# Optimization experiments

Measured on AMD Instinct MI355X. Metric: run time of the kernel, lower is better.

Reference implementation:

```python
import jax, jax.numpy as jnp
import numpy as np

DIM = 1024
CTX_DIM = 1024
HEADS = 8
DIM_HEAD = 64
INNER = HEADS * DIM_HEAD  # 512
EPS = 1e-5


def _layer_norm(x, gamma, beta):
    mu = jnp.mean(x, axis=-1, keepdims=True)
    var = jnp.mean(jnp.square(x - mu), axis=-1, keepdims=True)
    return (x - mu) * jax.lax.rsqrt(var + EPS) * gamma + beta


def setup_inputs() -> dict:
    key = jax.random.key(0)
    ks = jax.random.split(key, 8)
    b, n, m = 4, 2048, 2048
    x = jax.random.normal(ks[0], (b, n, DIM), dtype=jnp.float32)
    context = jax.random.normal(ks[1], (b, m, CTX_DIM), dtype=jnp.float32)
    Wq = jax.random.normal(ks[2], (DIM, INNER), dtype=jnp.float32) / np.sqrt(DIM)
    Wkv = jax.random.normal(ks[3], (CTX_DIM, 2 * INNER), dtype=jnp.float32) / np.sqrt(CTX_DIM)
    Wout = jax.random.normal(ks[4], (INNER, DIM), dtype=jnp.float32) / np.sqrt(INNER)
    bout = jnp.zeros((DIM,), dtype=jnp.float32)
    g1 = jnp.ones((DIM,), dtype=jnp.float32)
    b1 = jnp.zeros((DIM,), dtype=jnp.float32)
    g2 = jnp.ones((CTX_DIM,), dtype=jnp.float32)
    b2 = jnp.zeros((CTX_DIM,), dtype=jnp.float32)
    return {"x": x, "context": context, "g1": g1, "b1": b1, "g2": g2, "b2": b2,
            "Wq": Wq, "Wkv": Wkv, "Wout": Wout, "bout": bout}


def reference(x, context, g1, b1, g2, b2, Wq, Wkv, Wout, bout):
    b, n, _ = x.shape
    m = context.shape[1]
    scale = DIM_HEAD ** -0.5
    xn = _layer_norm(x, g1, b1)
    cn = _layer_norm(context, g2, b2)
    q = xn @ Wq                      # [b, n, inner]
    kv = cn @ Wkv                    # [b, m, 2*inner]
    k, v = jnp.split(kv, 2, axis=-1)
    # split heads: [b, h, seq, d]
    q = q.reshape(b, n, HEADS, DIM_HEAD).transpose(0, 2, 1, 3)
    k = k.reshape(b, m, HEADS, DIM_HEAD).transpose(0, 2, 1, 3)
    v = v.reshape(b, m, HEADS, DIM_HEAD).transpose(0, 2, 1, 3)
    sim = jnp.einsum('bhid,bhjd->bhij', q, k) * scale
    attn = jax.nn.softmax(sim, axis=-1)
    out = jnp.einsum('bhij,bhjd->bhid', attn, v)
    out = out.transpose(0, 2, 1, 3).reshape(b, n, INNER)
    return out @ Wout + bout
```

## Files before the change

kernel.cpp:

```cpp
#include <hip/hip_runtime.h>
#include <hip/hip_bf16.h>

typedef __bf16 bf16_t;
typedef bf16_t bf16x4 __attribute__((ext_vector_type(4)));
typedef bf16_t bf16x8 __attribute__((ext_vector_type(8)));
typedef float floatx4 __attribute__((ext_vector_type(4)));

typedef __attribute__((address_space(1))) const unsigned char* gptr_t;
typedef __attribute__((address_space(3))) unsigned char* lptr_t;

#define BATCH 4
#define SEQ_N 2048
#define SEQ_M 2048
#define DIM 1024
#define INNER 512
#define HEADS 8
#define DHEAD 64
#define QSCALE 0.18033688011112042f

#if __has_builtin(__builtin_amdgcn_exp2f)
#define fast_exp2(x) __builtin_amdgcn_exp2f(x)
#else
#define fast_exp2(x) exp2f(x)
#endif

__device__ __forceinline__ void wtrans_tile(const float* W, bf16_t* Wt,
                                            int K, int N, int n0, int k0, float scale) {
    __shared__ bf16_t T[64][72];
    const int tid = threadIdx.x;
#pragma unroll
    for (int p = 0; p < 2; p++) {
        int r = (tid >> 3) + p * 32;
        int c = (tid & 7) * 8;
        const float* src = W + (size_t)(k0 + r) * N + n0 + c;
        float4 v0 = *(const float4*)src;
        float4 v1 = *(const float4*)(src + 4);
        T[r][c + 0] = (bf16_t)(v0.x * scale); T[r][c + 1] = (bf16_t)(v0.y * scale);
        T[r][c + 2] = (bf16_t)(v0.z * scale); T[r][c + 3] = (bf16_t)(v0.w * scale);
        T[r][c + 4] = (bf16_t)(v1.x * scale); T[r][c + 5] = (bf16_t)(v1.y * scale);
        T[r][c + 6] = (bf16_t)(v1.z * scale); T[r][c + 7] = (bf16_t)(v1.w * scale);
    }
    __syncthreads();
#pragma unroll
    for (int p = 0; p < 2; p++) {
        int rn = (tid >> 3) + p * 32;
        int ck = (tid & 7) * 8;
        bf16x8 v;
#pragma unroll
        for (int i = 0; i < 8; i++) v[i] = T[ck + i][rn];
        *(bf16x8*)(Wt + (size_t)(n0 + rn) * K + k0 + ck) = v;
    }
}

__device__ __forceinline__ void ln_row_wave(const float* in, const float* g,
                                            const float* bt, bf16_t* out, int row) {
    const int lane = threadIdx.x & 63;
    const float4* src = (const float4*)(in + (size_t)row * 1024);
    float4 xv[4];
    float s = 0.f, ss = 0.f;
#pragma unroll
    for (int k = 0; k < 4; k++) {
        xv[k] = src[lane + k * 64];
        s  += xv[k].x + xv[k].y + xv[k].z + xv[k].w;
        ss += xv[k].x * xv[k].x + xv[k].y * xv[k].y + xv[k].z * xv[k].z + xv[k].w * xv[k].w;
    }
#pragma unroll
    for (int off = 32; off > 0; off >>= 1) {
        s  += __shfl_down(s, off);
        ss += __shfl_down(ss, off);
    }
    s  = __shfl(s, 0);
    ss = __shfl(ss, 0);
    const float mu = s * (1.f / 1024.f);
    const float var = ss * (1.f / 1024.f) - mu * mu;
    const float rs = rsqrtf(var + 1e-5f);
    const float4* gp = (const float4*)g;
    const float4* bp = (const float4*)bt;
#pragma unroll
    for (int k = 0; k < 4; k++) {
        float4 gv = gp[lane + k * 64], bv = bp[lane + k * 64];
        bf16x4 o;
        o[0] = (bf16_t)((xv[k].x - mu) * rs * gv.x + bv.x);
        o[1] = (bf16_t)((xv[k].y - mu) * rs * gv.y + bv.y);
        o[2] = (bf16_t)((xv[k].z - mu) * rs * gv.z + bv.z);
        o[3] = (bf16_t)((xv[k].w - mu) * rs * gv.w + bv.w);
        *(bf16x4*)(out + (size_t)row * 1024 + (lane + k * 64) * 4) = o;
    }
}

__global__ __launch_bounds__(256) void prep_kernel(const float* __restrict__ x,
                                                   const float* __restrict__ ctx,
                                                   const float* __restrict__ g1,
                                                   const float* __restrict__ b1,
                                                   const float* __restrict__ g2,
                                                   const float* __restrict__ b2,
                                                   const float* __restrict__ Wq,
                                                   const float* __restrict__ Wkv,
                                                   const float* __restrict__ Wout,
                                                   bf16_t* __restrict__ xn,
                                                   bf16_t* __restrict__ cn,
                                                   bf16_t* __restrict__ Wqt,
                                                   bf16_t* __restrict__ Wkvt,
                                                   bf16_t* __restrict__ Woutt) {
    int id = blockIdx.x;
    if (id < 128) {
        wtrans_tile(Wq, Wqt, 1024, 512, (id & 7) * 64, (id >> 3) * 64, QSCALE);
    } else if (id < 384) {
        int t = id - 128;
        wtrans_tile(Wkv, Wkvt, 1024, 1024, (t & 15) * 64, (t >> 4) * 64, 1.0f);
    } else if (id < 512) {
        int t = id - 384;
        wtrans_tile(Wout, Woutt, 512, 1024, (t & 15) * 64, (t >> 4) * 64, 1.0f);
    } else {
        int row = (id - 512) * 4 + (threadIdx.x >> 6);
        if (row < BATCH * SEQ_N) ln_row_wave(x, g1, b1, xn, row);
        else                     ln_row_wave(ctx, g2, b2, cn, row - BATCH * SEQ_N);
    }
}

template <int NT, int MODE, typename OutT>
__device__ __forceinline__ void gemm_body(const bf16_t* __restrict__ A,
                                          const bf16_t* __restrict__ Bt,
                                          OutT* __restrict__ C,
                                          const float* __restrict__ bias,
                                          int ldC, int K, int row0, int col0) {
    __shared__ bf16_t As[128 * 64];
    __shared__ bf16_t Bs[NT * 64];
    const int tid = threadIdx.x;
    const int wave = tid >> 6, lane = tid & 63;
    constexpr int WC = NT / 2;
    constexpr int NJ = WC / 16;
    const int wr = (wave >> 1) * 64, wc = (wave & 1) * WC;
    const int quad = lane >> 4, l16 = lane & 15;

    floatx4 acc[4][NJ] = {};

    for (int k0 = 0; k0 < K; k0 += 64) {
#pragma unroll
        for (int p = 0; p < 4; p++) {
            int cA = p * 256 + wave * 64 + lane;
            int rA = cA >> 3, kc = (cA & 7) * 8;
            __builtin_amdgcn_global_load_lds(
                (gptr_t)(A + (size_t)(row0 + rA) * K + k0 + kc),
                (lptr_t)(As + (size_t)(p * 256 + wave * 64) * 8), 16, 0, 0);
            if (p < NT / 32)
                __builtin_amdgcn_global_load_lds(
                    (gptr_t)(Bt + (size_t)(col0 + rA) * K + k0 + kc),
                    (lptr_t)(Bs + (size_t)(p * 256 + wave * 64) * 8), 16, 0, 0);
        }
        __syncthreads();
#pragma unroll
        for (int kt = 0; kt < 2; kt++) {
            bf16x8 aF[4], bF[NJ];
#pragma unroll
            for (int i = 0; i < 4; i++)
                aF[i] = *(bf16x8*)&As[(wr + i * 16 + l16) * 64 + kt * 32 + quad * 8];
#pragma unroll
            for (int j = 0; j < NJ; j++)
                bF[j] = *(bf16x8*)&Bs[(wc + j * 16 + l16) * 64 + kt * 32 + quad * 8];
#pragma unroll
            for (int i = 0; i < 4; i++)
#pragma unroll
                for (int j = 0; j < NJ; j++) {
                    if (MODE == 0)
                        acc[i][j] = __builtin_amdgcn_mfma_f32_16x16x32_bf16(
                            aF[i], bF[j], acc[i][j], 0, 0, 0);
                    else
                        acc[i][j] = __builtin_amdgcn_mfma_f32_16x16x32_bf16(
                            bF[j], aF[i], acc[i][j], 0, 0, 0);
                }
        }
        __syncthreads();
    }

    if (MODE == 0) {
#pragma unroll
        for (int i = 0; i < 4; i++)
#pragma unroll
            for (int j = 0; j < NJ; j++) {
                int col = col0 + wc + j * 16 + l16;
                float bv = bias ? bias[col] : 0.f;
#pragma unroll
                for (int r = 0; r < 4; r++) {
                    int row = row0 + wr + i * 16 + quad * 4 + r;
                    C[(size_t)row * ldC + col] = (OutT)(acc[i][j][r] + bv);
                }
            }
    } else {
        bf16_t* Tw = (wave < 2 ? As : Bs) + (wave & 1) * 4096;
#pragma unroll
        for (int i = 0; i < 4; i++)
#pragma unroll
            for (int j = 0; j < 4; j++)
#pragma unroll
                for (int r = 0; r < 4; r++)
                    Tw[(j * 16 + quad * 4 + r) * 64 + i * 16 + l16] = (bf16_t)acc[i][j][r];
        __syncthreads();
        const int grow = row0 + wr;
        const int bat = grow >> 11, gm = (grow & 2047) + l16 * 4;
#pragma unroll
        for (int dd = 0; dd < 16; dd++) {
            int d = dd * 4 + quad;
            bf16x4 v = *(bf16x4*)&Tw[d * 64 + l16 * 4];
            int gd = col0 + wc + d - 512;
            *(bf16x4*)(C + ((size_t)bat * 512 + gd) * 2048 + gm) = v;
        }
    }
}

__global__ __launch_bounds__(256) void gemm_qkv_kernel(const bf16_t* __restrict__ xn,
                                                       const bf16_t* __restrict__ cn,
                                                       const bf16_t* __restrict__ Wqt,
                                                       const bf16_t* __restrict__ Wkvt,
                                                       bf16_t* __restrict__ qb,
                                                       bf16_t* __restrict__ kvb,
                                                       bf16_t* __restrict__ Vtg) {
    const int bx = blockIdx.x;
    const int row0 = blockIdx.y * 128;
    if (bx < 4)
        gemm_body<128, 0, bf16_t>(xn, Wqt, qb, nullptr, 512, DIM, row0, bx * 128);
    else if (bx < 8)
        gemm_body<128, 0, bf16_t>(cn, Wkvt, kvb, nullptr, 512, DIM, row0, (bx - 4) * 128);
    else
        gemm_body<128, 1, bf16_t>(cn, Wkvt, Vtg, nullptr, 0, DIM, row0, (bx - 4) * 128);
}

__global__ __launch_bounds__(256) void gemm_out_kernel(const bf16_t* __restrict__ ao,
                                                       const bf16_t* __restrict__ Woutt,
                                                       float* __restrict__ out,
                                                       const float* __restrict__ bias) {
    gemm_body<64, 0, float>(ao, Woutt, out, bias, DIM, INNER,
                            blockIdx.y * 128, blockIdx.x * 64);
}

__global__ __launch_bounds__(128) void attn_kernel(const bf16_t* __restrict__ q,
                                                   const bf16_t* __restrict__ kv,
                                                   const bf16_t* __restrict__ Vtg,
                                                   bf16_t* __restrict__ o) {
    __shared__ bf16_t Qs[64 * 64];
    __shared__ bf16_t Ks[2][64 * 64];
    __shared__ bf16_t Vs[2][64 * 64];

    const int f = blockIdx.x;
    const int lb = ((f & 7) << 7) | (f >> 3);
    const int b = lb >> 8, h = (lb >> 5) & 7;
    const int n0 = (lb & 31) * 64;

    const int tid = threadIdx.x;
    const int wave = tid >> 6, lane = tid & 63;
    const int quad = lane >> 4, l16 = lane & 15;
    const int swz = (l16 & 7) << 3;

    const int sr = tid >> 3;
    const int sc = (tid & 7) * 8;
    const int scs = sc ^ ((sr & 7) << 3);

#pragma unroll
    for (int p = 0; p < 4; p++) {
        int r = sr + p * 16;
        *(bf16x8*)&Qs[r * 64 + scs] =
            *(const bf16x8*)(q + (size_t)(b * SEQ_N + n0 + r) * INNER + h * DHEAD + sc);
    }

    bf16x8 bOnes;
    {
        bf16_t ov = (l16 == 0) ? (bf16_t)1.0f : (bf16_t)0.0f;
#pragma unroll
        for (int i = 0; i < 8; i++) bOnes[i] = ov;
    }

    const bf16_t* kp = kv + (size_t)(b * SEQ_M) * 512 + h * DHEAD + sc;
    const bf16_t* vp = Vtg + (size_t)((b * HEADS + h) * DHEAD) * SEQ_M + sc;
    bf16x8 kreg[4], vreg[4];
#pragma unroll
    for (int p = 0; p < 4; p++) {
        kreg[p] = *(const bf16x8*)(kp + (size_t)(sr + p * 16) * 512);
        vreg[p] = *(const bf16x8*)(vp + (size_t)(sr + p * 16) * SEQ_M);
    }
    __syncthreads();

    bf16x8 aQ0[2], aQ1[2];
#pragma unroll
    for (int kt = 0; kt < 2; kt++) {
        aQ0[kt] = *(bf16x8*)&Qs[(wave * 32 + l16) * 64 + ((kt * 32 + quad * 8) ^ swz)];
        aQ1[kt] = *(bf16x8*)&Qs[(wave * 32 + 16 + l16) * 64 + ((kt * 32 + quad * 8) ^ swz)];
    }

#pragma unroll
    for (int p = 0; p < 4; p++) {
        int r = sr + p * 16;
        *(bf16x8*)&Ks[0][r * 64 + scs] = kreg[p];
        *(bf16x8*)&Vs[0][r * 64 + scs] = vreg[p];
    }
    kp += 64 * 512;
    vp += 64;
#pragma unroll
    for (int p = 0; p < 4; p++) {
        kreg[p] = *(const bf16x8*)(kp + (size_t)(sr + p * 16) * 512);
        vreg[p] = *(const bf16x8*)(vp + (size_t)(sr + p * 16) * SEQ_M);
    }
    __syncthreads();

    bf16_t* Pw0 = Qs + wave * 2048;
    bf16_t* Pw1 = Pw0 + 1024;

    floatx4 oacc0[5] = {}, oacc1[5] = {};

    int cur = 0;
    for (int it = 0; it < SEQ_M / 64; ++it) {
#pragma unroll
        for (int p = 0; p < 4; p++) {
            int r = sr + p * 16;
            *(bf16x8*)&Ks[cur ^ 1][r * 64 + scs] = kreg[p];
            *(bf16x8*)&Vs[cur ^ 1][r * 64 + scs] = vreg[p];
        }
        kp += 64 * 512;
        vp += 64;
#pragma unroll
        for (int p = 0; p < 4; p++) {
            kreg[p] = *(const bf16x8*)(kp + (size_t)(sr + p * 16) * 512);
            vreg[p] = *(const bf16x8*)(vp + (size_t)(sr + p * 16) * SEQ_M);
        }

        floatx4 s0[4] = {}, s1[4] = {};
#pragma unroll
        for (int kt = 0; kt < 2; kt++)
#pragma unroll
            for (int jt = 0; jt < 4; jt++) {
                bf16x8 aK = *(bf16x8*)&Ks[cur][(jt * 16 + l16) * 64 +
                                              ((kt * 32 + quad * 8) ^ swz)];
                s0[jt] = __builtin_amdgcn_mfma_f32_16x16x32_bf16(aK, aQ0[kt], s0[jt], 0, 0, 0);
                s1[jt] = __builtin_amdgcn_mfma_f32_16x16x32_bf16(aK, aQ1[kt], s1[jt], 0, 0, 0);
            }

#pragma unroll
        for (int jt = 0; jt < 4; jt++) {
            bf16x4 pk0, pk1;
#pragma unroll
            for (int r = 0; r < 4; r++) {
                pk0[r] = (bf16_t)fast_exp2(s0[jt][r]);
                pk1[r] = (bf16_t)fast_exp2(s1[jt][r]);
            }
            int pc = (jt * 16 + quad * 4) ^ swz;
            *(bf16x4*)&Pw0[l16 * 64 + pc] = pk0;
            *(bf16x4*)&Pw1[l16 * 64 + pc] = pk1;
        }

#pragma unroll
        for (int kt = 0; kt < 2; kt++) {
            int ac = (kt * 32 + quad * 8) ^ swz;
            bf16x8 aP0 = *(bf16x8*)&Pw0[l16 * 64 + ac];
            bf16x8 aP1 = *(bf16x8*)&Pw1[l16 * 64 + ac];
#pragma unroll
            for (int dt = 0; dt < 4; dt++) {
                bf16x8 bV = *(bf16x8*)&Vs[cur][(dt * 16 + l16) * 64 + ac];
                oacc0[dt] = __builtin_amdgcn_mfma_f32_16x16x32_bf16(aP0, bV, oacc0[dt], 0, 0, 0);
                oacc1[dt] = __builtin_amdgcn_mfma_f32_16x16x32_bf16(aP1, bV, oacc1[dt], 0, 0, 0);
            }
            oacc0[4] = __builtin_amdgcn_mfma_f32_16x16x32_bf16(aP0, bOnes, oacc0[4], 0, 0, 0);
            oacc1[4] = __builtin_amdgcn_mfma_f32_16x16x32_bf16(aP1, bOnes, oacc1[4], 0, 0, 0);
        }
        __syncthreads();
        cur ^= 1;
    }

#pragma unroll
    for (int set = 0; set < 2; set++) {
        const floatx4* oa = set == 0 ? oacc0 : oacc1;
        float inv[4];
#pragma unroll
        for (int r = 0; r < 4; r++) {
            float l = __shfl(oa[4][r], (int)(lane & 48));
            inv[r] = 1.0f / l;
        }
#pragma unroll
        for (int dt = 0; dt < 4; dt++)
#pragma unroll
            for (int r = 0; r < 4; r++) {
                int row = n0 + wave * 32 + set * 16 + quad * 4 + r;
                int col = h * DHEAD + dt * 16 + l16;
                o[(size_t)(b * SEQ_N + row) * INNER + col] =
                    (bf16_t)(oa[dt][r] * inv[r]);
            }
    }
}

extern "C" void kernel_launch(void* const* d_in, const int* in_sizes, int n_in,
                              void* d_out, int out_size, void* d_ws, size_t ws_size,
                              hipStream_t stream) {
    const float* x    = (const float*)d_in[0];
    const float* ctx  = (const float*)d_in[1];
    const float* g1   = (const float*)d_in[2];
    const float* b1   = (const float*)d_in[3];
    const float* g2   = (const float*)d_in[4];
    const float* b2   = (const float*)d_in[5];
    const float* Wq   = (const float*)d_in[6];
    const float* Wkv  = (const float*)d_in[7];
    const float* Wout = (const float*)d_in[8];
    const float* bout = (const float*)d_in[9];
    float* out = (float*)d_out;

    const int rows = BATCH * SEQ_N;
    bf16_t* xn    = (bf16_t*)d_ws;
    bf16_t* cn    = xn + (size_t)rows * DIM;
    bf16_t* qb    = cn + (size_t)rows * DIM;
    bf16_t* kvb   = qb + (size_t)rows * INNER;
    bf16_t* Vtg   = kvb + (size_t)rows * INNER;
    bf16_t* Wqt   = Vtg + (size_t)rows * INNER;
    bf16_t* Wkvt  = Wqt + (size_t)INNER * DIM;
    bf16_t* Woutt = Wkvt + (size_t)(2 * INNER) * DIM;
    bf16_t* o_attn = xn;

    prep_kernel<<<512 + (2 * rows) / 4, 256, 0, stream>>>(
        x, ctx, g1, b1, g2, b2, Wq, Wkv, Wout, xn, cn, Wqt, Wkvt, Woutt);
    gemm_qkv_kernel<<<dim3(12, rows / 128), 256, 0, stream>>>(
        xn, cn, Wqt, Wkvt, qb, kvb, Vtg);
    attn_kernel<<<dim3(SEQ_N / 64 * HEADS * BATCH), 128, 0, stream>>>(qb, kvb, Vtg, o_attn);
    gemm_out_kernel<<<dim3(DIM / 64, rows / 128), 256, 0, stream>>>(o_attn, Woutt, out, bout);
}
```

Measured before the change: 245.1 us.

## Stream K via direct global-to-LDS loads, read V from global, remap GEMM blocks

The attention kernel now loads K tiles straight into LDS with global_load_lds and an XOR-swizzled source column, replacing the register-staged copy. The V shared buffer is removed: V fragments come from global memory (L2) directly into registers for the PV MFMAs. Both GEMM kernels get 1D grids with XCD-aware block remapping, and attention gets a launch-bounds occupancy hint. This cuts LDS traffic, LDS footprint and register staging, at the cost of V global-load latency inside the loop and reliance on L2 hits.

New measurement: 262.5 us. 1.07x slower.

```diff
diff --git a/kernel.cpp b/kernel.cpp
--- a/kernel.cpp
+++ b/kernel.cpp
@@ -215,8 +215,10 @@
                                                        bf16_t* __restrict__ qb,
                                                        bf16_t* __restrict__ kvb,
                                                        bf16_t* __restrict__ Vtg) {
-    const int bx = blockIdx.x;
-    const int row0 = blockIdx.y * 128;
+    const int f = blockIdx.x;
+    const int lb = (f & 7) * 96 + (f >> 3);
+    const int bx = lb % 12;
+    const int row0 = (lb / 12) * 128;
     if (bx < 4)
         gemm_body<128, 0, bf16_t>(xn, Wqt, qb, nullptr, 512, DIM, row0, bx * 128);
     else if (bx < 8)
@@ -229,17 +231,18 @@
                                                        const bf16_t* __restrict__ Woutt,
                                                        float* __restrict__ out,
                                                        const float* __restrict__ bias) {
+    const int f = blockIdx.x;
+    const int lb = (f & 7) * 128 + (f >> 3);
     gemm_body<64, 0, float>(ao, Woutt, out, bias, DIM, INNER,
-                            blockIdx.y * 128, blockIdx.x * 64);
-}
-
-__global__ __launch_bounds__(128) void attn_kernel(const bf16_t* __restrict__ q,
-                                                   const bf16_t* __restrict__ kv,
-                                                   const bf16_t* __restrict__ Vtg,
-                                                   bf16_t* __restrict__ o) {
+                            (lb >> 4) * 128, (lb & 15) * 64);
+}
+
+__global__ __launch_bounds__(128, 3) void attn_kernel(const bf16_t* __restrict__ q,
+                                                      const bf16_t* __restrict__ kv,
+                                                      const bf16_t* __restrict__ Vtg,
+                                                      bf16_t* __restrict__ o) {
     __shared__ bf16_t Qs[64 * 64];
     __shared__ bf16_t Ks[2][64 * 64];
-    __shared__ bf16_t Vs[2][64 * 64];
 
     const int f = blockIdx.x;
     const int lb = ((f & 7) << 7) | (f >> 3);
@@ -255,6 +258,17 @@
     const int sc = (tid & 7) * 8;
     const int scs = sc ^ ((sr & 7) << 3);
 
+    const int rloc = lane >> 3;
+    const int srccol = ((lane & 7) ^ rloc) << 3;
+    const bf16_t* kgl = kv + ((size_t)(b * SEQ_M) + wave * 32 + rloc) * 512
+                           + h * DHEAD + srccol;
+
+#pragma unroll
+    for (int p = 0; p < 4; p++)
+        __builtin_amdgcn_global_load_lds(
+            (gptr_t)(kgl + (size_t)(p * 8) * 512),
+            (lptr_t)(Ks[0] + (wave * 4 + p) * 512), 16, 0, 0);
+
 #pragma unroll
     for (int p = 0; p < 4; p++) {
         int r = sr + p * 16;
@@ -269,14 +283,6 @@
         for (int i = 0; i < 8; i++) bOnes[i] = ov;
     }
 
-    const bf16_t* kp = kv + (size_t)(b * SEQ_M) * 512 + h * DHEAD + sc;
-    const bf16_t* vp = Vtg + (size_t)((b * HEADS + h) * DHEAD) * SEQ_M + sc;
-    bf16x8 kreg[4], vreg[4];
-#pragma unroll
-    for (int p = 0; p < 4; p++) {
-        kreg[p] = *(const bf16x8*)(kp + (size_t)(sr + p * 16) * 512);
-        vreg[p] = *(const bf16x8*)(vp + (size_t)(sr + p * 16) * SEQ_M);
-    }
     __syncthreads();
 
     bf16x8 aQ0[2], aQ1[2];
@@ -286,20 +292,15 @@
         aQ1[kt] = *(bf16x8*)&Qs[(wave * 32 + 16 + l16) * 64 + ((kt * 32 + quad * 8) ^ swz)];
     }
 
-#pragma unroll
-    for (int p = 0; p < 4; p++) {
-        int r = sr + p * 16;
-        *(bf16x8*)&Ks[0][r * 64 + scs] = kreg[p];
-        *(bf16x8*)&Vs[0][r * 64 + scs] = vreg[p];
-    }
-    kp += 64 * 512;
-    vp += 64;
-#pragma unroll
-    for (int p = 0; p < 4; p++) {
-        kreg[p] = *(const bf16x8*)(kp + (size_t)(sr + p * 16) * 512);
-        vreg[p] = *(const bf16x8*)(vp + (size_t)(sr + p * 16) * SEQ_M);
-    }
-    __syncthreads();
+    kgl += (size_t)64 * 512;
+#pragma unroll
+    for (int p = 0; p < 4; p++)
+        __builtin_amdgcn_global_load_lds(
+            (gptr_t)(kgl + (size_t)(p * 8) * 512),
+            (lptr_t)(Ks[1] + (wave * 4 + p) * 512), 16, 0, 0);
+
+    const bf16_t* vbl =
+        Vtg + ((size_t)((b * HEADS + h) * DHEAD) + l16) * SEQ_M + quad * 8;
 
     bf16_t* Pw0 = Qs + wave * 2048;
     bf16_t* Pw1 = Pw0 + 1024;
@@ -308,20 +309,6 @@
 
     int cur = 0;
     for (int it = 0; it < SEQ_M / 64; ++it) {
-#pragma unroll
-        for (int p = 0; p < 4; p++) {
-            int r = sr + p * 16;
-            *(bf16x8*)&Ks[cur ^ 1][r * 64 + scs] = kreg[p];
-            *(bf16x8*)&Vs[cur ^ 1][r * 64 + scs] = vreg[p];
-        }
-        kp += 64 * 512;
-        vp += 64;
-#pragma unroll
-        for (int p = 0; p < 4; p++) {
-            kreg[p] = *(const bf16x8*)(kp + (size_t)(sr + p * 16) * 512);
-            vreg[p] = *(const bf16x8*)(vp + (size_t)(sr + p * 16) * SEQ_M);
-        }
-
         floatx4 s0[4] = {}, s1[4] = {};
 #pragma unroll
         for (int kt = 0; kt < 2; kt++)
@@ -333,6 +320,11 @@
                 s1[jt] = __builtin_amdgcn_mfma_f32_16x16x32_bf16(aK, aQ1[kt], s1[jt], 0, 0, 0);
             }
 
+        bf16x8 vf0[4], vf1[4];
+#pragma unroll
+        for (int dt = 0; dt < 4; dt++)
+            vf0[dt] = *(const bf16x8*)(vbl + (size_t)(dt * 16) * SEQ_M);
+
 #pragma unroll
         for (int jt = 0; jt < 4; jt++) {
             bf16x4 pk0, pk1;
@@ -347,20 +339,42 @@
         }
 
 #pragma unroll
-        for (int kt = 0; kt < 2; kt++) {
-            int ac = (kt * 32 + quad * 8) ^ swz;
+        for (int dt = 0; dt < 4; dt++)
+            vf1[dt] = *(const bf16x8*)(vbl + (size_t)(dt * 16) * SEQ_M + 32);
+
+        {
+            int ac = (quad * 8) ^ swz;
             bf16x8 aP0 = *(bf16x8*)&Pw0[l16 * 64 + ac];
             bf16x8 aP1 = *(bf16x8*)&Pw1[l16 * 64 + ac];
 #pragma unroll
             for (int dt = 0; dt < 4; dt++) {
-                bf16x8 bV = *(bf16x8*)&Vs[cur][(dt * 16 + l16) * 64 + ac];
-                oacc0[dt] = __builtin_amdgcn_mfma_f32_16x16x32_bf16(aP0, bV, oacc0[dt], 0, 0, 0);
-                oacc1[dt] = __builtin_amdgcn_mfma_f32_16x16x32_bf16(aP1, bV, oacc1[dt], 0, 0, 0);
+                oacc0[dt] = __builtin_amdgcn_mfma_f32_16x16x32_bf16(aP0, vf0[dt], oacc0[dt], 0, 0, 0);
+                oacc1[dt] = __builtin_amdgcn_mfma_f32_16x16x32_bf16(aP1, vf0[dt], oacc1[dt], 0, 0, 0);
             }
             oacc0[4] = __builtin_amdgcn_mfma_f32_16x16x32_bf16(aP0, bOnes, oacc0[4], 0, 0, 0);
             oacc1[4] = __builtin_amdgcn_mfma_f32_16x16x32_bf16(aP1, bOnes, oacc1[4], 0, 0, 0);
-        }
+
+            ac = (32 + quad * 8) ^ swz;
+            aP0 = *(bf16x8*)&Pw0[l16 * 64 + ac];
+            aP1 = *(bf16x8*)&Pw1[l16 * 64 + ac];
+#pragma unroll
+            for (int dt = 0; dt < 4; dt++) {
+                oacc0[dt] = __builtin_amdgcn_mfma_f32_16x16x32_bf16(aP0, vf1[dt], oacc0[dt], 0, 0, 0);
+                oacc1[dt] = __builtin_amdgcn_mfma_f32_16x16x32_bf16(aP1, vf1[dt], oacc1[dt], 0, 0, 0);
+            }
+            oacc0[4] = __builtin_amdgcn_mfma_f32_16x16x32_bf16(aP0, bOnes, oacc0[4], 0, 0, 0);
+            oacc1[4] = __builtin_amdgcn_mfma_f32_16x16x32_bf16(aP1, bOnes, oacc1[4], 0, 0, 0);
+        }
+        vbl += 64;
+
         __syncthreads();
+
+        kgl += (size_t)64 * 512;
+#pragma unroll
+        for (int p = 0; p < 4; p++)
+            __builtin_amdgcn_global_load_lds(
+                (gptr_t)(kgl + (size_t)(p * 8) * 512),
+                (lptr_t)(Ks[cur] + (wave * 4 + p) * 512), 16, 0, 0);
         cur ^= 1;
     }
 
@@ -413,8 +427,8 @@
 
     prep_kernel<<<512 + (2 * rows) / 4, 256, 0, stream>>>(
         x, ctx, g1, b1, g2, b2, Wq, Wkv, Wout, xn, cn, Wqt, Wkvt, Woutt);
-    gemm_qkv_kernel<<<dim3(12, rows / 128), 256, 0, stream>>>(
+    gemm_qkv_kernel<<<768, 256, 0, stream>>>(
         xn, cn, Wqt, Wkvt, qb, kvb, Vtg);
-    attn_kernel<<<dim3(SEQ_N / 64 * HEADS * BATCH), 128, 0, stream>>>(qb, kvb, Vtg, o_attn);
-    gemm_out_kernel<<<dim3(DIM / 64, rows / 128), 256, 0, stream>>>(o_attn, Woutt, out, bout);
-}
+    attn_kernel<<<1024, 128, 0, stream>>>(qb, kvb, Vtg, o_attn);
+    gemm_out_kernel<<<1024, 256, 0, stream>>>(o_attn, Woutt, out, bout);
+}
```
